# Kernel optimization log

Measured on AMD Instinct MI355X. Metric: run time of the kernel, lower is better.

Reference implementation:

```python
import jax, jax.numpy as jnp
import numpy as np

V, D, DFF, E, K, L = 32000, 1024, 4096, 8, 2, 2
B, S = 2, 1024


def _layer_norm(x, scale, bias, eps=1e-5):
    mu = jnp.mean(x, axis=-1, keepdims=True)
    var = jnp.var(x, axis=-1, keepdims=True)
    return (x - mu) * jax.lax.rsqrt(var + eps) * scale + bias


def setup_inputs() -> dict:
    key = jax.random.key(0)
    ks = jax.random.split(key, 16)
    s = 0.02
    return {
        "input_ids": jax.random.randint(ks[0], (B, S), 0, V, dtype=jnp.int32),
        "emb": jax.random.normal(ks[1], (V, D), jnp.float32) * s,
        "t_ln_scale": jnp.ones((L, D), jnp.float32),
        "t_ln_bias": jnp.zeros((L, D), jnp.float32),
        "t_w1": jax.random.normal(ks[2], (L, D, DFF), jnp.float32) * s,
        "t_b1": jnp.zeros((L, DFF), jnp.float32),
        "t_w2": jax.random.normal(ks[3], (L, DFF, D), jnp.float32) * s,
        "t_b2": jnp.zeros((L, D), jnp.float32),
        "Wr": jax.random.normal(ks[4], (D, E), jnp.float32) * s,
        "br": jnp.zeros((E,), jnp.float32),
        "e_w1": jax.random.normal(ks[5], (E, D, DFF), jnp.float32) * s,
        "e_b1": jnp.zeros((E, DFF), jnp.float32),
        "e_w2": jax.random.normal(ks[6], (E, DFF, D), jnp.float32) * s,
        "e_b2": jnp.zeros((E, D), jnp.float32),
        "Wl": jax.random.normal(ks[7], (D, V), jnp.float32) * s,
        "bl": jnp.zeros((V,), jnp.float32),
    }


def reference(input_ids, emb, t_ln_scale, t_ln_bias, t_w1, t_b1, t_w2, t_b2,
              Wr, br, e_w1, e_b1, e_w2, e_b2, Wl, bl):
    # token embeddings: [B,S,D]
    x = emb[input_ids]

    # temporal abstraction: L pre-LN residual MLP blocks
    for l in range(L):
        h = _layer_norm(x, t_ln_scale[l], t_ln_bias[l])
        h = jax.nn.gelu(jnp.einsum('bsd,df->bsf', h, t_w1[l]) + t_b1[l])
        x = x + jnp.einsum('bsf,fd->bsd', h, t_w2[l]) + t_b2[l]

    # router: top-k renormalized softmax over experts, scattered to [B,S,E]
    r_logits = jnp.einsum('bsd,de->bse', x, Wr) + br
    top_vals, top_idx = jax.lax.top_k(r_logits, K)
    top_w = jax.nn.softmax(top_vals, axis=-1)
    routing_weights = jnp.put_along_axis(
        jnp.zeros_like(r_logits), top_idx, top_w, axis=-1, inplace=False)

    # dense all-experts stack: [B,S,E,D]
    h = jax.nn.gelu(jnp.einsum('bsd,edf->bsef', x, e_w1) + e_b1)
    expert_out = jnp.einsum('bsef,efd->bsed', h, e_w2) + e_b2

    # sparse-weighted combine
    y = jnp.einsum('bse,bsed->bsd', routing_weights, expert_out)

    logits = jnp.einsum('bsd,dv->bsv', y, Wl) + bl
    return logits, routing_weights
```

## Files before the change

### kernel.cpp

```cpp
#include <hip/hip_runtime.h>
#include <stdint.h>

typedef __bf16 bf16;
typedef __bf16 bf16x8 __attribute__((ext_vector_type(8)));
typedef float f32x4 __attribute__((ext_vector_type(4)));

#define DEV __device__ __forceinline__

static constexpr int Dm   = 1024;
static constexpr int DFFm = 4096;
static constexpr int Tm   = 2048;
static constexpr int Vm   = 32000;

#define GLOAD_LDS16(g, l)                                                      \
  __builtin_amdgcn_global_load_lds(                                            \
      (const __attribute__((address_space(1))) unsigned int*)(g),              \
      (__attribute__((address_space(3))) unsigned int*)(l), 16, 0, 0)

DEV float gelu_tanh(float v) {
  float u = 0.7978845608028654f * (v + 0.044715f * v * v * v);
  float e = __expf(2.0f * u);
  float t = 1.0f - 2.0f / (e + 1.0f);
  return 0.5f * v * (1.0f + t);
}

enum { EPI_GELU_SPLIT = 0, EPI_RESID = 1, EPI_GELU_BF16 = 2, EPI_MOE = 3, EPI_BIAS = 4 };

struct GemmP {
  const bf16* Ah;
  const bf16* Bh;
  const float* bias;
  const float* rwp;
  const int* cnt;
  const int* idx;
  float* outF;
  bf16* outH;
  int K; int N;
  int lda; int ldb; int ldo;
  long aBS, bBS, outBS;
  int biasBS;
  int ebase;
  int kcShift; int kcK;
};

template <int EPI, bool GATHER, bool SWZ>
__launch_bounds__(256, 2)
__global__ void gemm_bt(GemmP p) {
  __shared__ bf16 lds[16384];
  bf16* ldsA = lds;
  bf16* ldsB = lds + 8192;

  const int tid  = threadIdx.x;
  const int lane = tid & 63;
  const int wid  = tid >> 6;
  const int wr   = wid >> 1;
  const int wc   = wid & 1;
  const int z    = blockIdx.z;
  const int kc   = z & ((1 << p.kcShift) - 1);
  const int ze   = z >> p.kcShift;

  int bx = blockIdx.x, by = blockIdx.y;
  if constexpr (SWZ) {
    const int gx = gridDim.x, gy = gridDim.y;
    const int nwg = gx * gy;
    const int lin = by * gx + bx;
    const int q = nwg >> 3, r = nwg & 7;
    const int xcd = lin & 7, loc = lin >> 3;
    const int nid = (xcd < r ? xcd * (q + 1) : r * (q + 1) + (xcd - r) * q) + loc;
    bx = nid / gy; by = nid % gy;
  }

  const long am0 = (long)by * 128;
  const long bn0 = (long)bx * 128;

  int cntE = 0;
  const int* il = nullptr;
  if constexpr (GATHER || EPI == EPI_MOE) {
    cntE = p.cnt[p.ebase + ze];
    if (am0 >= cntE) return;
    il = p.idx + (long)(p.ebase + ze) * 2048;
  }

  const long lda = p.lda, ldb = p.ldb;
  const long K = p.K;
  const long kco = (long)kc * p.kcK;

  const int sub = (lane & 7) ^ (lane >> 3);
  const int rIn = wid * 8 + (lane >> 3);

  const bf16 *aS[4], *bS[4];
  {
    const bf16* Bb = p.Bh + (long)ze * p.bBS + kco + bn0 * ldb;
    const bf16* Ab = p.Ah + (long)ze * p.aBS + kco + am0 * lda;
#pragma unroll
    for (int j = 0; j < 4; ++j) {
      const int row = j * 32 + rIn;
      bS[j] = Bb + (long)row * ldb + sub * 8;
      if constexpr (GATHER) {
        const int rt = (int)am0 + row;
        const long grow = il[rt < cntE ? rt : 0];
        aS[j] = p.Ah + grow * lda + kco + sub * 8;
      } else {
        aS[j] = Ab + (long)row * lda + sub * 8;
      }
    }
  }
  char* dstA[4];
#pragma unroll
  for (int j = 0; j < 4; ++j)
    dstA[j] = (char*)(void*)lds + (j * 256 + wid * 64) * 16;

  f32x4 acc[4][4] = {};

  const int r15 = lane & 15;
  const int kcs = lane >> 4;
  const int xk  = lane & 7;

  for (long k0 = 0; k0 < K; k0 += 64) {
    __syncthreads();
#pragma unroll
    for (int j = 0; j < 4; ++j) {
      GLOAD_LDS16(aS[j] + k0, dstA[j]);
      GLOAD_LDS16(bS[j] + k0, dstA[j] + 16384);
    }
    __syncthreads();
#pragma unroll
    for (int h = 0; h < 2; ++h) {
      const int q8 = ((kcs + 4 * h) ^ xk) << 3;
      bf16x8 a[4], b[4];
#pragma unroll
      for (int m = 0; m < 4; ++m)
        a[m] = *(const bf16x8*)(ldsA + (wr * 64 + m * 16 + r15) * 64 + q8);
#pragma unroll
      for (int n = 0; n < 4; ++n)
        b[n] = *(const bf16x8*)(ldsB + (wc * 64 + n * 16 + r15) * 64 + q8);
#pragma unroll
      for (int m = 0; m < 4; ++m)
#pragma unroll
        for (int n = 0; n < 4; ++n)
          acc[m][n] = __builtin_amdgcn_mfma_f32_16x16x32_bf16(a[m], b[n], acc[m][n], 0, 0, 0);
    }
  }

  const long N = p.N;

#pragma unroll
  for (int m = 0; m < 4; ++m) {
#pragma unroll
    for (int n = 0; n < 4; ++n) {
      const long col = bn0 + wc * 64 + n * 16 + (lane & 15);
      const float bv = (kc == 0) ? p.bias[(long)ze * p.biasBS + col] : 0.0f;
#pragma unroll
      for (int r = 0; r < 4; ++r) {
        const long row = am0 + wr * 64 + m * 16 + (lane >> 4) * 4 + r;
        float v = acc[m][n][r] + bv;
        if constexpr (EPI == EPI_GELU_SPLIT) {
          float g = gelu_tanh(v);
          bf16 hh = (bf16)g;
          long o = row * (long)p.ldo + col;
          p.outH[o] = hh;
          p.outH[o + N] = (bf16)(g - (float)hh);
          p.outH[o + 2 * N] = hh;
        } else if constexpr (EPI == EPI_RESID) {
          atomicAdd(p.outF + row * N + col, v);
        } else if constexpr (EPI == EPI_GELU_BF16) {
          long o = (long)ze * p.outBS + row * N + col;
          p.outH[o] = (bf16)gelu_tanh(v);
        } else if constexpr (EPI == EPI_MOE) {
          if (row < cntE) {
            const int tok = il[row];
            const float wgt = p.rwp[(long)tok * 8 + p.ebase + ze];
            atomicAdd(p.outF + (long)tok * N + col, wgt * v);
          }
        } else {
          p.outF[row * N + col] = v;
        }
      }
    }
  }
}

template <bool AUG>
__global__ void transpose_cvt(const float* __restrict__ in, bf16* __restrict__ out,
                              int R, int C, long inBS, long outBS) {
  __shared__ float tile[32][33];
  const float* inp = in + (long)blockIdx.z * inBS;
  const long c0 = (long)blockIdx.x * 32;
  const long r0 = (long)blockIdx.y * 32;
  const int tx = threadIdx.x;
  const int ty = threadIdx.y;
#pragma unroll
  for (int i = 0; i < 4; ++i) {
    int r = ty + i * 8;
    tile[r][tx] = inp[(r0 + r) * (long)C + c0 + tx];
  }
  __syncthreads();
  const long ob = (long)blockIdx.z * outBS;
  const long stride = AUG ? 3L * R : (long)R;
#pragma unroll
  for (int i = 0; i < 4; ++i) {
    int c = ty + i * 8;
    float v = tile[tx][c];
    bf16 h = (bf16)v;
    long o = ob + (c0 + c) * stride + r0 + tx;
    out[o] = h;
    if constexpr (AUG) {
      out[o + R] = h;
      out[o + 2 * R] = (bf16)(v - (float)h);
    }
  }
}

__global__ void embed_kernel(const int* __restrict__ ids, const float* __restrict__ emb,
                             float* __restrict__ x) {
  const long t = blockIdx.x;
  const int id = ids[t];
  ((float4*)(x + t * 1024))[threadIdx.x] = ((const float4*)(emb + (long)id * 1024))[threadIdx.x];
}

__global__ void ln_aug_kernel(const float* __restrict__ x, const float* __restrict__ sc,
                              const float* __restrict__ bi, bf16* __restrict__ oa) {
  const long t = blockIdx.x;
  const int tid = threadIdx.x;
  const int lane = tid & 63, wid = tid >> 6;
  float4 a = ((const float4*)(x + t * 1024))[tid];
  float s = a.x + a.y + a.z + a.w;
  float q = a.x * a.x + a.y * a.y + a.z * a.z + a.w * a.w;
#pragma unroll
  for (int off = 32; off; off >>= 1) {
    s += __shfl_down(s, off);
    q += __shfl_down(q, off);
  }
  __shared__ float sr[4], qr[4];
  if (lane == 0) { sr[wid] = s; qr[wid] = q; }
  __syncthreads();
  s = sr[0] + sr[1] + sr[2] + sr[3];
  q = qr[0] + qr[1] + qr[2] + qr[3];
  const float mu = s * (1.0f / 1024.0f);
  const float var = q * (1.0f / 1024.0f) - mu * mu;
  const float rs = rsqrtf(var + 1e-5f);
#pragma unroll
  for (int j = 0; j < 4; ++j) {
    const int d = tid * 4 + j;
    const float g = (((const float*)&a)[j] - mu) * rs * sc[d] + bi[d];
    const bf16 h = (bf16)g;
    oa[t * 3072 + d] = h;
    oa[t * 3072 + 1024 + d] = (bf16)(g - (float)h);
    oa[t * 3072 + 2048 + d] = h;
  }
}

__global__ void router_kernel(const float* __restrict__ x, const float* __restrict__ Wr,
                              const float* __restrict__ br, float* __restrict__ rwo,
                              int* __restrict__ top2) {
  const long t = blockIdx.x;
  const int lane = threadIdx.x;
  float acc[8];
#pragma unroll
  for (int e = 0; e < 8; ++e) acc[e] = 0.0f;
  const float4* xr = (const float4*)(x + t * 1024);
#pragma unroll
  for (int j = 0; j < 4; ++j) {
    const int d4 = j * 64 + lane;
    float4 xv = xr[d4];
#pragma unroll
    for (int u = 0; u < 4; ++u) {
      const float xs = ((const float*)&xv)[u];
      const float4* wp = (const float4*)(Wr + (long)(d4 * 4 + u) * 8);
      float4 w0 = wp[0], w1 = wp[1];
      acc[0] += xs * w0.x; acc[1] += xs * w0.y; acc[2] += xs * w0.z; acc[3] += xs * w0.w;
      acc[4] += xs * w1.x; acc[5] += xs * w1.y; acc[6] += xs * w1.z; acc[7] += xs * w1.w;
    }
  }
#pragma unroll
  for (int off = 32; off; off >>= 1)
#pragma unroll
    for (int e = 0; e < 8; ++e) acc[e] += __shfl_down(acc[e], off);
  if (lane == 0) {
    float v[8];
#pragma unroll
    for (int e = 0; e < 8; ++e) v[e] = acc[e] + br[e];
    int i0 = 0; float v0 = v[0];
    for (int e = 1; e < 8; ++e) if (v[e] > v0) { v0 = v[e]; i0 = e; }
    int i1 = -1; float v1 = -3.4e38f;
    for (int e = 0; e < 8; ++e) if (e != i0 && v[e] > v1) { v1 = v[e]; i1 = e; }
    float e1 = expf(v1 - v0);
    float den = 1.0f + e1;
    float w0 = 1.0f / den, w1 = e1 / den;
    float* o = rwo + t * 8;
#pragma unroll
    for (int e = 0; e < 8; ++e) o[e] = (e == i0) ? w0 : (e == i1 ? w1 : 0.0f);
    top2[t] = i0 | (i1 << 8);
  }
}

__global__ void build_lists(const int* __restrict__ top2, int* __restrict__ cnt,
                            int* __restrict__ idx) {
  const int t = blockIdx.x * 256 + threadIdx.x;
  const int rec = top2[t];
  const int e0 = rec & 255, e1 = (rec >> 8) & 255;
  int p0 = atomicAdd(&cnt[e0], 1);
  idx[e0 * 2048 + p0] = t;
  int p1 = atomicAdd(&cnt[e1], 1);
  idx[e1 * 2048 + p1] = t;
}

__global__ void cvt_bf16_kernel(const float* __restrict__ in, bf16* __restrict__ out, long n) {
  long i = ((long)blockIdx.x * blockDim.x + threadIdx.x) * 8;
  if (i >= n) return;
  float4 a = *(const float4*)(in + i);
  float4 b = *(const float4*)(in + i + 4);
  bf16x8 o;
  o[0] = (bf16)a.x; o[1] = (bf16)a.y; o[2] = (bf16)a.z; o[3] = (bf16)a.w;
  o[4] = (bf16)b.x; o[5] = (bf16)b.y; o[6] = (bf16)b.z; o[7] = (bf16)b.w;
  *(bf16x8*)(out + i) = o;
}

extern "C" void kernel_launch(void* const* d_in, const int* in_sizes, int n_in,
                              void* d_out, int out_size, void* d_ws, size_t ws_size,
                              hipStream_t stream) {
  (void)in_sizes; (void)n_in; (void)out_size; (void)ws_size;
  const int*   ids  = (const int*)d_in[0];
  const float* emb  = (const float*)d_in[1];
  const float* tlns = (const float*)d_in[2];
  const float* tlnb = (const float*)d_in[3];
  const float* tw1  = (const float*)d_in[4];
  const float* tb1  = (const float*)d_in[5];
  const float* tw2  = (const float*)d_in[6];
  const float* tb2  = (const float*)d_in[7];
  const float* Wr   = (const float*)d_in[8];
  const float* br   = (const float*)d_in[9];
  const float* ew1  = (const float*)d_in[10];
  const float* eb1  = (const float*)d_in[11];
  const float* ew2  = (const float*)d_in[12];
  const float* eb2  = (const float*)d_in[13];
  const float* Wl   = (const float*)d_in[14];
  const float* bl   = (const float*)d_in[15];

  float* logits = (float*)d_out;
  float* rwout  = (float*)d_out + (long)Tm * Vm;

  size_t off = 0;
  auto take = [&](size_t bytes) {
    void* pp = (char*)d_ws + off;
    off += (bytes + 255) & ~(size_t)255;
    return pp;
  };
  float* X    = (float*)take((size_t)Tm * Dm * 4);
  bf16*  XB   = (bf16*) take((size_t)Tm * Dm * 2);
  float* Y    = (float*)take((size_t)Tm * Dm * 4);
  bf16*  YB   = (bf16*) take((size_t)Tm * Dm * 2);
  int*   top2 = (int*)  take((size_t)Tm * 4);
  int*   cnt  = (int*)  take(8 * 4);
  int*   idxl = (int*)  take((size_t)8 * Tm * 4);
  char*  S    = (char*) take(134217728);

  bf16* A1  = (bf16*)S;
  bf16* W1A = (bf16*)(S + 12582912);
  bf16* W2A = (bf16*)(S + 12582912 + 25165824);
  bf16* HTA = (bf16*)(S + 12582912 + 2 * 25165824);
  bf16* EW1T = (bf16*)S;
  bf16* HE   = (bf16*)(S + 33554432);
  bf16* EW2T = (bf16*)(S + 100663296);
  bf16* WLT  = (bf16*)S;

  embed_kernel<<<dim3(Tm), dim3(256), 0, stream>>>(ids, emb, X);

  for (int l = 0; l < 2; ++l) {
    transpose_cvt<true><<<dim3(DFFm / 32, Dm / 32, 1), dim3(32, 8), 0, stream>>>(
        tw1 + (long)l * Dm * DFFm, W1A, Dm, DFFm, 0, 0);
    transpose_cvt<true><<<dim3(Dm / 32, DFFm / 32, 1), dim3(32, 8), 0, stream>>>(
        tw2 + (long)l * DFFm * Dm, W2A, DFFm, Dm, 0, 0);
    ln_aug_kernel<<<dim3(Tm), dim3(256), 0, stream>>>(X, tlns + l * Dm, tlnb + l * Dm, A1);

    GemmP p1{};
    p1.Ah = A1; p1.Bh = W1A;
    p1.bias = tb1 + (long)l * DFFm;
    p1.outH = HTA;
    p1.K = 3072; p1.N = DFFm; p1.lda = 3072; p1.ldb = 3072; p1.ldo = 3 * DFFm;
    gemm_bt<EPI_GELU_SPLIT, false, true>
        <<<dim3(DFFm / 128, Tm / 128, 1), dim3(256), 0, stream>>>(p1);

    GemmP p2{};
    p2.Ah = HTA; p2.Bh = W2A;
    p2.bias = tb2 + (long)l * Dm;
    p2.outF = X;
    p2.K = 1536; p2.N = Dm; p2.lda = 12288; p2.ldb = 12288;
    p2.kcShift = 3; p2.kcK = 1536;
    gemm_bt<EPI_RESID, false, true>
        <<<dim3(Dm / 128, Tm / 128, 8), dim3(256), 0, stream>>>(p2);
  }

  router_kernel<<<dim3(Tm), dim3(64), 0, stream>>>(X, Wr, br, rwout, top2);
  hipMemsetAsync(cnt, 0, 8 * 4, stream);
  build_lists<<<dim3(Tm / 256), dim3(256), 0, stream>>>(top2, cnt, idxl);
  cvt_bf16_kernel<<<dim3(Tm * Dm / (256 * 8)), dim3(256), 0, stream>>>(X, XB, (long)Tm * Dm);
  hipMemsetAsync(Y, 0, (size_t)Tm * Dm * 4, stream);

  for (int q = 0; q < 2; ++q) {
    transpose_cvt<false><<<dim3(DFFm / 32, Dm / 32, 4), dim3(32, 8), 0, stream>>>(
        ew1 + (long)q * 4 * Dm * DFFm, EW1T, Dm, DFFm, (long)Dm * DFFm, (long)DFFm * Dm);
    transpose_cvt<false><<<dim3(Dm / 32, DFFm / 32, 4), dim3(32, 8), 0, stream>>>(
        ew2 + (long)q * 4 * DFFm * Dm, EW2T, DFFm, Dm, (long)DFFm * Dm, (long)Dm * DFFm);

    GemmP pe1{};
    pe1.Ah = XB; pe1.Bh = EW1T;
    pe1.bias = eb1 + (long)q * 4 * DFFm; pe1.biasBS = DFFm;
    pe1.outH = HE; pe1.outBS = (long)Tm * DFFm;
    pe1.aBS = 0; pe1.bBS = (long)DFFm * Dm;
    pe1.cnt = cnt; pe1.idx = idxl; pe1.ebase = q * 4;
    pe1.K = Dm; pe1.N = DFFm; pe1.lda = Dm; pe1.ldb = Dm;
    gemm_bt<EPI_GELU_BF16, true, true>
        <<<dim3(DFFm / 128, Tm / 128, 4), dim3(256), 0, stream>>>(pe1);

    GemmP pe2{};
    pe2.Ah = HE; pe2.aBS = (long)Tm * DFFm;
    pe2.Bh = EW2T; pe2.bBS = (long)Dm * DFFm;
    pe2.bias = eb2 + (long)q * 4 * Dm; pe2.biasBS = Dm;
    pe2.rwp = rwout; pe2.cnt = cnt; pe2.idx = idxl; pe2.ebase = q * 4;
    pe2.outF = Y;
    pe2.K = 1024; pe2.N = Dm; pe2.lda = DFFm; pe2.ldb = DFFm;
    pe2.kcShift = 2; pe2.kcK = 1024;
    gemm_bt<EPI_MOE, false, true>
        <<<dim3(Dm / 128, Tm / 128, 16), dim3(256), 0, stream>>>(pe2);
  }

  cvt_bf16_kernel<<<dim3(Tm * Dm / (256 * 8)), dim3(256), 0, stream>>>(Y, YB, (long)Tm * Dm);
  transpose_cvt<false><<<dim3(Vm / 32, Dm / 32, 1), dim3(32, 8), 0, stream>>>(
      Wl, WLT, Dm, Vm, 0, 0);
  GemmP pl{};
  pl.Ah = YB; pl.Bh = WLT; pl.bias = bl;
  pl.outF = logits;
  pl.K = Dm; pl.N = Vm; pl.lda = Dm; pl.ldb = Dm;
  gemm_bt<EPI_BIAS, false, true>
      <<<dim3(Vm / 128, Tm / 128, 1), dim3(256), 0, stream>>>(pl);
}
```

Measured before the change: 1.007 ms.

## Triple-buffer GEMM K loop, drop duplicated split copies, fuse router with list build

The GEMM main loop now uses a three-stage LDS ring with 32-wide K steps, issuing loads two tiles ahead and managing them with explicit vmcnt waits. It also raises MFMA priority and targets three blocks per CU. The bf16 hi/lo split operands are stored as two copies instead of three, with the third K segment remapped by index wraparound, which cuts memory traffic in the temporal MLP GEMMs. Weight transposes use 64x64 tiles with float4 loads and bf16x4 stores. The router now also does the bf16 conversion of X and builds the per-expert token lists, removing two kernels. Risks include register pressure at higher occupancy and nondeterministic list order from the atomics.

```diff
diff --git a/kernel.cpp b/kernel.cpp
--- a/kernel.cpp
+++ b/kernel.cpp
@@ -3,6 +3,7 @@
 
 typedef __bf16 bf16;
 typedef __bf16 bf16x8 __attribute__((ext_vector_type(8)));
+typedef __bf16 bf16x4 __attribute__((ext_vector_type(4)));
 typedef float f32x4 __attribute__((ext_vector_type(4)));
 
 #define DEV __device__ __forceinline__
@@ -41,14 +42,13 @@
   int biasBS;
   int ebase;
   int kcShift; int kcK;
+  int aT, aS2, bT, bS2;
 };
 
 template <int EPI, bool GATHER, bool SWZ>
-__launch_bounds__(256, 2)
+__launch_bounds__(256, 3)
 __global__ void gemm_bt(GemmP p) {
-  __shared__ bf16 lds[16384];
-  bf16* ldsA = lds;
-  bf16* ldsB = lds + 8192;
+  __shared__ bf16 lds[24576];
 
   const int tid  = threadIdx.x;
   const int lane = tid & 63;
@@ -82,68 +82,87 @@
   }
 
   const long lda = p.lda, ldb = p.ldb;
-  const long K = p.K;
+  const int NT = p.K >> 5;
   const long kco = (long)kc * p.kcK;
 
-  const int sub = (lane & 7) ^ (lane >> 3);
-  const int rIn = wid * 8 + (lane >> 3);
-
-  const bf16 *aS[4], *bS[4];
+  const int row0 = wid * 16 + (lane >> 2);
+  const int gk8  = (((lane & 3) ^ ((lane >> 3) & 3))) * 8;
+  const bf16 *aS0, *aS1, *bS0, *bS1;
   {
-    const bf16* Bb = p.Bh + (long)ze * p.bBS + kco + bn0 * ldb;
-    const bf16* Ab = p.Ah + (long)ze * p.aBS + kco + am0 * lda;
-#pragma unroll
-    for (int j = 0; j < 4; ++j) {
-      const int row = j * 32 + rIn;
-      bS[j] = Bb + (long)row * ldb + sub * 8;
-      if constexpr (GATHER) {
-        const int rt = (int)am0 + row;
-        const long grow = il[rt < cntE ? rt : 0];
-        aS[j] = p.Ah + grow * lda + kco + sub * 8;
-      } else {
-        aS[j] = Ab + (long)row * lda + sub * 8;
-      }
+    const bf16* Bb = p.Bh + (long)ze * p.bBS + bn0 * ldb;
+    bS0 = Bb + (long)row0 * ldb + gk8;
+    bS1 = Bb + (long)(row0 + 64) * ldb + gk8;
+    if constexpr (GATHER) {
+      const int rt0 = (int)am0 + row0;
+      const int rt1 = rt0 + 64;
+      const long g0 = il[rt0 < cntE ? rt0 : 0];
+      const long g1 = il[rt1 < cntE ? rt1 : 0];
+      aS0 = p.Ah + g0 * lda + gk8;
+      aS1 = p.Ah + g1 * lda + gk8;
+    } else {
+      const bf16* Ab = p.Ah + (long)ze * p.aBS + am0 * lda;
+      aS0 = Ab + (long)row0 * lda + gk8;
+      aS1 = Ab + (long)(row0 + 64) * lda + gk8;
     }
   }
-  char* dstA[4];
-#pragma unroll
-  for (int j = 0; j < 4; ++j)
-    dstA[j] = (char*)(void*)lds + (j * 256 + wid * 64) * 16;
+  char* ldsc = (char*)(void*)lds;
+  const int woff = wid * 1024;
+
+  auto stage = [&](int t, int buf) {
+    const long kv = kco + (long)t * 32;
+    const long ka = (kv >= p.aT) ? kv - p.aS2 : kv;
+    const long kb = (kv >= p.bT) ? kv - p.bS2 : kv;
+    char* base = ldsc + buf * 16384;
+    GLOAD_LDS16(aS0 + ka, base + woff);
+    GLOAD_LDS16(aS1 + ka, base + 4096 + woff);
+    GLOAD_LDS16(bS0 + kb, base + 8192 + woff);
+    GLOAD_LDS16(bS1 + kb, base + 12288 + woff);
+  };
 
   f32x4 acc[4][4] = {};
-
   const int r15 = lane & 15;
   const int kcs = lane >> 4;
-  const int xk  = lane & 7;
-
-  for (long k0 = 0; k0 < K; k0 += 64) {
-    __syncthreads();
-#pragma unroll
-    for (int j = 0; j < 4; ++j) {
-      GLOAD_LDS16(aS[j] + k0, dstA[j]);
-      GLOAD_LDS16(bS[j] + k0, dstA[j] + 16384);
+  const int q8  = ((kcs ^ ((r15 >> 1) & 3))) << 3;
+
+  stage(0, 0);
+  if (NT > 1) stage(1, 1);
+
+  int cur = 0;
+  for (int t = 0; t < NT; ++t) {
+    __builtin_amdgcn_s_barrier();
+    if (t + 2 < NT) {
+      stage(t + 2, cur == 0 ? 2 : cur - 1);
+      asm volatile("s_waitcnt vmcnt(8)" ::: "memory");
+    } else if (t + 1 < NT) {
+      asm volatile("s_waitcnt vmcnt(4)" ::: "memory");
+    } else {
+      asm volatile("s_waitcnt vmcnt(0)" ::: "memory");
     }
-    __syncthreads();
-#pragma unroll
-    for (int h = 0; h < 2; ++h) {
-      const int q8 = ((kcs + 4 * h) ^ xk) << 3;
-      bf16x8 a[4], b[4];
-#pragma unroll
-      for (int m = 0; m < 4; ++m)
-        a[m] = *(const bf16x8*)(ldsA + (wr * 64 + m * 16 + r15) * 64 + q8);
+    __builtin_amdgcn_s_barrier();
+
+    const bf16* bufA = lds + cur * 8192;
+    const bf16* bufB = bufA + 4096;
+
+    bf16x8 a[4], b[4];
+#pragma unroll
+    for (int m = 0; m < 4; ++m)
+      a[m] = *(const bf16x8*)(bufA + (wr * 64 + m * 16 + r15) * 32 + q8);
+#pragma unroll
+    for (int n = 0; n < 4; ++n)
+      b[n] = *(const bf16x8*)(bufB + (wc * 64 + n * 16 + r15) * 32 + q8);
+
+    __builtin_amdgcn_s_setprio(1);
+#pragma unroll
+    for (int m = 0; m < 4; ++m)
 #pragma unroll
       for (int n = 0; n < 4; ++n)
-        b[n] = *(const bf16x8*)(ldsB + (wc * 64 + n * 16 + r15) * 64 + q8);
-#pragma unroll
-      for (int m = 0; m < 4; ++m)
-#pragma unroll
-        for (int n = 0; n < 4; ++n)
-          acc[m][n] = __builtin_amdgcn_mfma_f32_16x16x32_bf16(a[m], b[n], acc[m][n], 0, 0, 0);
-    }
+        acc[m][n] = __builtin_amdgcn_mfma_f32_16x16x32_bf16(a[m], b[n], acc[m][n], 0, 0, 0);
+    __builtin_amdgcn_s_setprio(0);
+
+    cur = (cur == 2) ? 0 : cur + 1;
   }
 
   const long N = p.N;
-
 #pragma unroll
   for (int m = 0; m < 4; ++m) {
 #pragma unroll
@@ -160,7 +179,6 @@
           long o = row * (long)p.ldo + col;
           p.outH[o] = hh;
           p.outH[o + N] = (bf16)(g - (float)hh);
-          p.outH[o + 2 * N] = hh;
         } else if constexpr (EPI == EPI_RESID) {
           atomicAdd(p.outF + row * N + col, v);
         } else if constexpr (EPI == EPI_GELU_BF16) {
@@ -183,31 +201,38 @@
 template <bool AUG>
 __global__ void transpose_cvt(const float* __restrict__ in, bf16* __restrict__ out,
                               int R, int C, long inBS, long outBS) {
-  __shared__ float tile[32][33];
+  __shared__ float tile[64][65];
   const float* inp = in + (long)blockIdx.z * inBS;
-  const long c0 = (long)blockIdx.x * 32;
-  const long r0 = (long)blockIdx.y * 32;
+  const long c0 = (long)blockIdx.x * 64;
+  const long r0 = (long)blockIdx.y * 64;
   const int tx = threadIdx.x;
   const int ty = threadIdx.y;
 #pragma unroll
   for (int i = 0; i < 4; ++i) {
-    int r = ty + i * 8;
-    tile[r][tx] = inp[(r0 + r) * (long)C + c0 + tx];
+    const int r = ty + i * 16;
+    const float4 v = *(const float4*)(inp + (r0 + r) * (long)C + c0 + tx * 4);
+    tile[r][tx * 4 + 0] = v.x;
+    tile[r][tx * 4 + 1] = v.y;
+    tile[r][tx * 4 + 2] = v.z;
+    tile[r][tx * 4 + 3] = v.w;
   }
   __syncthreads();
   const long ob = (long)blockIdx.z * outBS;
-  const long stride = AUG ? 3L * R : (long)R;
-#pragma unroll
-  for (int i = 0; i < 4; ++i) {
-    int c = ty + i * 8;
-    float v = tile[tx][c];
-    bf16 h = (bf16)v;
-    long o = ob + (c0 + c) * stride + r0 + tx;
-    out[o] = h;
-    if constexpr (AUG) {
-      out[o + R] = h;
-      out[o + 2 * R] = (bf16)(v - (float)h);
+  const long stride = AUG ? 2L * R : (long)R;
+#pragma unroll
+  for (int j = 0; j < 4; ++j) {
+    const int c = j * 16 + ty;
+    bf16x4 h, l;
+#pragma unroll
+    for (int u = 0; u < 4; ++u) {
+      float v = tile[tx * 4 + u][c];
+      bf16 hh = (bf16)v;
+      h[u] = hh;
+      if constexpr (AUG) l[u] = (bf16)(v - (float)hh);
     }
+    const long o = ob + (c0 + c) * stride + r0 + tx * 4;
+    *(bf16x4*)(out + o) = h;
+    if constexpr (AUG) *(bf16x4*)(out + o + R) = l;
   }
 }
 
@@ -218,8 +243,8 @@
   ((float4*)(x + t * 1024))[threadIdx.x] = ((const float4*)(emb + (long)id * 1024))[threadIdx.x];
 }
 
-__global__ void ln_aug_kernel(const float* __restrict__ x, const float* __restrict__ sc,
-                              const float* __restrict__ bi, bf16* __restrict__ oa) {
+__global__ void ln_aug2_kernel(const float* __restrict__ x, const float* __restrict__ sc,
+                               const float* __restrict__ bi, bf16* __restrict__ oa) {
   const long t = blockIdx.x;
   const int tid = threadIdx.x;
   const int lane = tid & 63, wid = tid >> 6;
@@ -244,15 +269,15 @@
     const int d = tid * 4 + j;
     const float g = (((const float*)&a)[j] - mu) * rs * sc[d] + bi[d];
     const bf16 h = (bf16)g;
-    oa[t * 3072 + d] = h;
-    oa[t * 3072 + 1024 + d] = (bf16)(g - (float)h);
-    oa[t * 3072 + 2048 + d] = h;
+    oa[t * 2048 + d] = h;
+    oa[t * 2048 + 1024 + d] = (bf16)(g - (float)h);
   }
 }
 
 __global__ void router_kernel(const float* __restrict__ x, const float* __restrict__ Wr,
                               const float* __restrict__ br, float* __restrict__ rwo,
-                              int* __restrict__ top2) {
+                              bf16* __restrict__ xb, int* __restrict__ cnt,
+                              int* __restrict__ idx) {
   const long t = blockIdx.x;
   const int lane = threadIdx.x;
   float acc[8];
@@ -263,6 +288,9 @@
   for (int j = 0; j < 4; ++j) {
     const int d4 = j * 64 + lane;
     float4 xv = xr[d4];
+    bf16x4 xh;
+    xh[0] = (bf16)xv.x; xh[1] = (bf16)xv.y; xh[2] = (bf16)xv.z; xh[3] = (bf16)xv.w;
+    *(bf16x4*)(xb + t * 1024 + (long)d4 * 4) = xh;
 #pragma unroll
     for (int u = 0; u < 4; ++u) {
       const float xs = ((const float*)&xv)[u];
@@ -290,19 +318,11 @@
     float* o = rwo + t * 8;
 #pragma unroll
     for (int e = 0; e < 8; ++e) o[e] = (e == i0) ? w0 : (e == i1 ? w1 : 0.0f);
-    top2[t] = i0 | (i1 << 8);
-  }
-}
-
-__global__ void build_lists(const int* __restrict__ top2, int* __restrict__ cnt,
-                            int* __restrict__ idx) {
-  const int t = blockIdx.x * 256 + threadIdx.x;
-  const int rec = top2[t];
-  const int e0 = rec & 255, e1 = (rec >> 8) & 255;
-  int p0 = atomicAdd(&cnt[e0], 1);
-  idx[e0 * 2048 + p0] = t;
-  int p1 = atomicAdd(&cnt[e1], 1);
-  idx[e1 * 2048 + p1] = t;
+    int p0 = atomicAdd(&cnt[i0], 1);
+    idx[i0 * 2048 + p0] = (int)t;
+    int p1 = atomicAdd(&cnt[i1], 1);
+    idx[i1 * 2048 + p1] = (int)t;
+  }
 }
 
 __global__ void cvt_bf16_kernel(const float* __restrict__ in, bf16* __restrict__ out, long n) {
@@ -350,15 +370,14 @@
   bf16*  XB   = (bf16*) take((size_t)Tm * Dm * 2);
   float* Y    = (float*)take((size_t)Tm * Dm * 4);
   bf16*  YB   = (bf16*) take((size_t)Tm * Dm * 2);
-  int*   top2 = (int*)  take((size_t)Tm * 4);
   int*   cnt  = (int*)  take(8 * 4);
   int*   idxl = (int*)  take((size_t)8 * Tm * 4);
   char*  S    = (char*) take(134217728);
 
   bf16* A1  = (bf16*)S;
-  bf16* W1A = (bf16*)(S + 12582912);
-  bf16* W2A = (bf16*)(S + 12582912 + 25165824);
-  bf16* HTA = (bf16*)(S + 12582912 + 2 * 25165824);
+  bf16* W1A = (bf16*)(S + 8388608);
+  bf16* W2A = (bf16*)(S + 25165824);
+  bf16* HTA = (bf16*)(S + 41943040);
   bf16* EW1T = (bf16*)S;
   bf16* HE   = (bf16*)(S + 33554432);
   bf16* EW2T = (bf16*)(S + 100663296);
@@ -367,17 +386,18 @@
   embed_kernel<<<dim3(Tm), dim3(256), 0, stream>>>(ids, emb, X);
 
   for (int l = 0; l < 2; ++l) {
-    transpose_cvt<true><<<dim3(DFFm / 32, Dm / 32, 1), dim3(32, 8), 0, stream>>>(
+    transpose_cvt<true><<<dim3(DFFm / 64, Dm / 64, 1), dim3(16, 16), 0, stream>>>(
         tw1 + (long)l * Dm * DFFm, W1A, Dm, DFFm, 0, 0);
-    transpose_cvt<true><<<dim3(Dm / 32, DFFm / 32, 1), dim3(32, 8), 0, stream>>>(
+    transpose_cvt<true><<<dim3(Dm / 64, DFFm / 64, 1), dim3(16, 16), 0, stream>>>(
         tw2 + (long)l * DFFm * Dm, W2A, DFFm, Dm, 0, 0);
-    ln_aug_kernel<<<dim3(Tm), dim3(256), 0, stream>>>(X, tlns + l * Dm, tlnb + l * Dm, A1);
+    ln_aug2_kernel<<<dim3(Tm), dim3(256), 0, stream>>>(X, tlns + l * Dm, tlnb + l * Dm, A1);
 
     GemmP p1{};
     p1.Ah = A1; p1.Bh = W1A;
     p1.bias = tb1 + (long)l * DFFm;
     p1.outH = HTA;
-    p1.K = 3072; p1.N = DFFm; p1.lda = 3072; p1.ldb = 3072; p1.ldo = 3 * DFFm;
+    p1.K = 3072; p1.N = DFFm; p1.lda = 2048; p1.ldb = 2048; p1.ldo = 2 * DFFm;
+    p1.aT = 2048; p1.aS2 = 2048; p1.bT = 1024; p1.bS2 = 1024;
     gemm_bt<EPI_GELU_SPLIT, false, true>
         <<<dim3(DFFm / 128, Tm / 128, 1), dim3(256), 0, stream>>>(p1);
 
@@ -385,22 +405,21 @@
     p2.Ah = HTA; p2.Bh = W2A;
     p2.bias = tb2 + (long)l * Dm;
     p2.outF = X;
-    p2.K = 1536; p2.N = Dm; p2.lda = 12288; p2.ldb = 12288;
+    p2.K = 1536; p2.N = Dm; p2.lda = 8192; p2.ldb = 8192;
     p2.kcShift = 3; p2.kcK = 1536;
+    p2.aT = 8192; p2.aS2 = 8192; p2.bT = 4096; p2.bS2 = 4096;
     gemm_bt<EPI_RESID, false, true>
         <<<dim3(Dm / 128, Tm / 128, 8), dim3(256), 0, stream>>>(p2);
   }
 
-  router_kernel<<<dim3(Tm), dim3(64), 0, stream>>>(X, Wr, br, rwout, top2);
   hipMemsetAsync(cnt, 0, 8 * 4, stream);
-  build_lists<<<dim3(Tm / 256), dim3(256), 0, stream>>>(top2, cnt, idxl);
-  cvt_bf16_kernel<<<dim3(Tm * Dm / (256 * 8)), dim3(256), 0, stream>>>(X, XB, (long)Tm * Dm);
+  router_kernel<<<dim3(Tm), dim3(64), 0, stream>>>(X, Wr, br, rwout, XB, cnt, idxl);
   hipMemsetAsync(Y, 0, (size_t)Tm * Dm * 4, stream);
 
   for (int q = 0; q < 2; ++q) {
-    transpose_cvt<false><<<dim3(DFFm / 32, Dm / 32, 4), dim3(32, 8), 0, stream>>>(
+    transpose_cvt<false><<<dim3(DFFm / 64, Dm / 64, 4), dim3(16, 16), 0, stream>>>(
         ew1 + (long)q * 4 * Dm * DFFm, EW1T, Dm, DFFm, (long)Dm * DFFm, (long)DFFm * Dm);
-    transpose_cvt<false><<<dim3(Dm / 32, DFFm / 32, 4), dim3(32, 8), 0, stream>>>(
+    transpose_cvt<false><<<dim3(Dm / 64, DFFm / 64, 4), dim3(16, 16), 0, stream>>>(
         ew2 + (long)q * 4 * DFFm * Dm, EW2T, DFFm, Dm, (long)DFFm * Dm, (long)Dm * DFFm);
 
     GemmP pe1{};
@@ -426,11 +445,10 @@
   }
 
   cvt_bf16_kernel<<<dim3(Tm * Dm / (256 * 8)), dim3(256), 0, stream>>>(Y, YB, (long)Tm * Dm);
-  transpose_cvt<false><<<dim3(Vm / 32, Dm / 32, 1), dim3(32, 8), 0, stream>>>(
+  transpose_cvt<false><<<dim3(Vm / 64, Dm / 64, 1), dim3(16, 16), 0, stream>>>(
       Wl, WLT, Dm, Vm, 0, 0);
   GemmP pl{};
-  pl.Ah = YB; pl.Bh = WLT; pl.bias = bl;
-  pl.outF = logits;
+  pl.Ah = YB; pl.Bh = WLT; pl.bias = bl; pl.outF = logits;
   pl.K = Dm; pl.N = Vm; pl.lda = Dm; pl.ldb = Dm;
   gemm_bt<EPI_BIAS, false, true>
       <<<dim3(Vm / 128, Tm / 128, 1), dim3(256), 0, stream>>>(pl);
```

After: 1.008 ms. About the same (+0.1%).
